# Performance work log

Measured on AMD Instinct MI355X. Metric: run time of the kernel, lower is better.

Reference implementation:

```python
import jax, jax.numpy as jnp
import numpy as np

D_IN = 768
D_OUT = 768
NUM_HEADS = 12
HEAD_DIM = D_OUT // NUM_HEADS


def setup_inputs() -> dict:
    key = jax.random.key(0)
    ks = jax.random.split(key, 9)
    s = 1.0 / np.sqrt(D_IN)
    x = jax.random.normal(ks[0], (8, 1024, D_IN), dtype=jnp.float32)
    Wq = jax.random.uniform(ks[1], (D_IN, D_OUT), jnp.float32, -s, s)
    Wk = jax.random.uniform(ks[2], (D_IN, D_OUT), jnp.float32, -s, s)
    Wv = jax.random.uniform(ks[3], (D_IN, D_OUT), jnp.float32, -s, s)
    Wo = jax.random.uniform(ks[4], (D_OUT, D_OUT), jnp.float32, -s, s)
    bq = jax.random.uniform(ks[5], (D_OUT,), jnp.float32, -s, s)
    bk = jax.random.uniform(ks[6], (D_OUT,), jnp.float32, -s, s)
    bv = jax.random.uniform(ks[7], (D_OUT,), jnp.float32, -s, s)
    bo = jax.random.uniform(ks[8], (D_OUT,), jnp.float32, -s, s)
    return {"x": x, "Wq": Wq, "bq": bq, "Wk": Wk, "bk": bk,
            "Wv": Wv, "bv": bv, "Wo": Wo, "bo": bo}


def reference(x, Wq, bq, Wk, bk, Wv, bv, Wo, bo):
    b, n, _ = x.shape
    # projections -> (b, heads, n, head_dim)
    def split_heads(t):
        return t.reshape(b, n, NUM_HEADS, HEAD_DIM).transpose(0, 2, 1, 3)
    q = split_heads(x @ Wq + bq)
    k = split_heads(x @ Wk + bk)
    v = split_heads(x @ Wv + bv)
    scale = 1.0 / jnp.sqrt(jnp.float32(HEAD_DIM)).astype(x.dtype)
    scores = jnp.einsum('bhqd,bhkd->bhqk', q, k) * scale
    attn = jax.nn.softmax(scores, axis=-1)  # dropout p=0.0 -> identity
    ctx = jnp.einsum('bhqk,bhkd->bhqd', attn, v)
    ctx = ctx.transpose(0, 2, 1, 3).reshape(b, n, D_OUT)
    return ctx @ Wo + bo
```

## Files before the change

### kernel.cpp

```cpp
#include <hip/hip_runtime.h>
#include <math.h>

#define D_MODEL 768
#define NHEAD  12
#define HDIM   64
#define SEQ    1024
#define BATCH  8
#define MTOT   (BATCH*SEQ)
#define QKV_N  2304
#define QK_LD  1536

typedef _Float16 f16;
typedef __attribute__((ext_vector_type(2))) __fp16 fp16x2;
typedef __attribute__((ext_vector_type(4))) _Float16 f16x4;
typedef __attribute__((ext_vector_type(8))) _Float16 f16x8;
typedef __attribute__((ext_vector_type(4))) float f32x4;
typedef __attribute__((ext_vector_type(16))) float f32x16;

union PFrag { unsigned u[4]; f16x8 v; };
union PackW { fp16x2 h; unsigned u; };

__device__ inline void gload_lds16(const void* g, void* l) {
    __builtin_amdgcn_global_load_lds(
        (const __attribute__((address_space(1))) void*)g,
        (__attribute__((address_space(3))) void*)l, 16, 0, 0);
}

__global__ __launch_bounds__(256) void prepass(
    const float* __restrict__ x, f16* __restrict__ xh, int n8,
    const float* __restrict__ bq, const float* __restrict__ bk,
    const float* __restrict__ bv, float* __restrict__ bqkv,
    const float* __restrict__ Wq, const float* __restrict__ Wk,
    const float* __restrict__ Wv, const float* __restrict__ Wo,
    f16* __restrict__ Wqkv_t, f16* __restrict__ Wo_t)
{
    __shared__ f16 tile[64][72];
    const int t = threadIdx.x;

    if (blockIdx.x < 3072) {
        const int i = blockIdx.x * 256 + t;
        if (i < n8) {
            const float4 a = *(const float4*)(x + (size_t)i * 8);
            const float4 b = *(const float4*)(x + (size_t)i * 8 + 4);
            f16x8 v;
            v[0] = (f16)a.x; v[1] = (f16)a.y; v[2] = (f16)a.z; v[3] = (f16)a.w;
            v[4] = (f16)b.x; v[5] = (f16)b.y; v[6] = (f16)b.z; v[7] = (f16)b.w;
            *(f16x8*)(xh + (size_t)i * 8) = v;
        }
        if (i < QKV_N)
            bqkv[i] = (i < 768) ? bq[i] : (i < 1536) ? bk[i - 768] : bv[i - 1536];
    } else {
        const int idx = blockIdx.x - 3072;
        const int z   = idx / 144;
        const int rem = idx % 144;
        const int k0  = (rem / 12) * 64;
        const int n0  = (rem % 12) * 64;
        const float* src = (z == 0) ? Wq : (z == 1) ? Wk : (z == 2) ? Wv : Wo;
        f16* dst = (z < 3) ? (Wqkv_t + (size_t)z * 768 * 768) : Wo_t;

        {
            const int r  = t >> 4;
            const int c4 = (t & 15) * 4;
            #pragma unroll
            for (int u = 0; u < 4; ++u) {
                const int row = r + u * 16;
                const float4 a = *(const float4*)&src[(size_t)(k0 + row) * 768 + n0 + c4];
                tile[row][c4 + 0] = (f16)a.x;
                tile[row][c4 + 1] = (f16)a.y;
                tile[row][c4 + 2] = (f16)a.z;
                tile[row][c4 + 3] = (f16)a.w;
            }
        }
        __syncthreads();
        {
            const int rn = t >> 3;
            const int ck = (t & 7) * 8;
            #pragma unroll
            for (int u = 0; u < 2; ++u) {
                const int n = rn + u * 32;
                f16x8 v;
                #pragma unroll
                for (int q = 0; q < 8; ++q) v[q] = tile[ck + q][n];
                *(f16x8*)&dst[(size_t)(n0 + n) * 768 + k0 + ck] = v;
            }
        }
    }
}

template<typename OUT_T, bool SPLITV, int BN>
__global__ __launch_bounds__(256) void gemm_f16_tn(
    const f16* __restrict__ A, const f16* __restrict__ Bt,
    const float* __restrict__ bias, OUT_T* __restrict__ C,
    f16* __restrict__ Vt,
    int M, int N, int K, int nb, int ldc)
{
    constexpr int NJ = BN / 32;
    __shared__ f16 As[128 * 64];
    __shared__ f16 Bs[BN * 64];

    const int t    = threadIdx.x;
    const int l15  = (t & 63) & 15;
    const int lg   = (t & 63) >> 4;
    const int w    = t >> 6;
    const int wrow = (w >> 1) * 64;
    const int wcol = (w & 1) * (BN / 2);

    const int orig = blockIdx.x;
    const int cpx  = gridDim.x >> 3;
    const int nid  = (orig & 7) * cpx + (orig >> 3);
    const int row0 = (nid / nb) * 128;
    const int col0 = (nid % nb) * BN;

    int src_row[4], src_koff[4], lds_off[4];
    #pragma unroll
    for (int i = 0; i < 4; ++i) {
        const int c = t + 256 * i;
        const int r = c >> 3;
        src_row[i]  = r;
        src_koff[i] = ((((c & 7) - (r >> 1)) & 7)) * 8;
        lds_off[i]  = c * 16;
    }

    int a_off[4][2], b_off[NJ][2];
    #pragma unroll
    for (int i = 0; i < 4; ++i) {
        const int ra = wrow + i * 16 + l15;
        #pragma unroll
        for (int s = 0; s < 2; ++s)
            a_off[i][s] = ra * 128 + (((s * 4 + lg + (ra >> 1)) & 7) * 16);
    }
    #pragma unroll
    for (int j = 0; j < NJ; ++j) {
        const int rb = wcol + j * 16 + l15;
        #pragma unroll
        for (int s = 0; s < 2; ++s)
            b_off[j][s] = rb * 128 + (((s * 4 + lg + (rb >> 1)) & 7) * 16);
    }

    f32x4 acc[4][NJ];
    #pragma unroll
    for (int i = 0; i < 4; ++i)
        #pragma unroll
        for (int j = 0; j < NJ; ++j)
            acc[i][j] = (f32x4){0.f, 0.f, 0.f, 0.f};

    const f16* Abase = A  + (size_t)row0 * K;
    const f16* Bbase = Bt + (size_t)col0 * K;

    for (int k0 = 0; k0 < K; k0 += 64) {
        #pragma unroll
        for (int i = 0; i < 4; ++i)
            gload_lds16(Abase + (size_t)src_row[i] * K + k0 + src_koff[i],
                        (char*)As + lds_off[i]);
        #pragma unroll
        for (int i = 0; i < BN / 32; ++i)
            gload_lds16(Bbase + (size_t)src_row[i] * K + k0 + src_koff[i],
                        (char*)Bs + lds_off[i]);
        __syncthreads();

        #pragma unroll
        for (int s = 0; s < 2; ++s) {
            f16x8 af[4], bf[NJ];
            #pragma unroll
            for (int i = 0; i < 4; ++i)
                af[i] = *(const f16x8*)((const char*)As + a_off[i][s]);
            #pragma unroll
            for (int j = 0; j < NJ; ++j)
                bf[j] = *(const f16x8*)((const char*)Bs + b_off[j][s]);
            #pragma unroll
            for (int i = 0; i < 4; ++i)
                #pragma unroll
                for (int j = 0; j < NJ; ++j)
                    acc[i][j] = __builtin_amdgcn_mfma_f32_16x16x32_f16(
                        af[i], bf[j], acc[i][j], 0, 0, 0);
        }
        __syncthreads();
    }

    #pragma unroll
    for (int j = 0; j < NJ; ++j) {
        const int col = col0 + wcol + j * 16 + l15;
        const float bj = bias[col];
        if (!SPLITV || col < 1536) {
            #pragma unroll
            for (int i = 0; i < 4; ++i) {
                const int row = row0 + wrow + i * 16 + lg * 4;
                #pragma unroll
                for (int q = 0; q < 4; ++q)
                    C[(size_t)(row + q) * ldc + col] = (OUT_T)(acc[i][j][q] + bj);
            }
        } else if (SPLITV) {
            const int h2 = (col - 1536) >> 6;
            const int d  = (col - 1536) & 63;
            #pragma unroll
            for (int i = 0; i < 4; ++i) {
                const int row = row0 + wrow + i * 16 + lg * 4;
                const int bb  = row >> 10;
                const int tok = row & 1023;
                f16x4 v4;
                #pragma unroll
                for (int q = 0; q < 4; ++q) v4[q] = (f16)(acc[i][j][q] + bj);
                *(f16x4*)(Vt + (((size_t)(bb * NHEAD + h2)) * 64 + d) * SEQ + tok) = v4;
            }
        }
    }
}

#define QMAP(r, hh) (((r) & 3) + 8 * ((r) >> 2) + 4 * (hh))

__global__ __launch_bounds__(256, 3) void attn_f16(
    const f16* __restrict__ QK, const f16* __restrict__ Vt,
    f16* __restrict__ O)
{
    __shared__ f16 KsB[2][64 * 64];
    __shared__ f16 VtB[2][64 * 64];

    const int t   = threadIdx.x;
    const int w   = t >> 6;
    const int l   = t & 63;
    const int l31 = l & 31;
    const int h   = l >> 5;
    const int sl  = (l & 7) << 4;

    const int orig = blockIdx.x;
    const int s    = (orig & 7) * 96 + (orig >> 3);
    const int bh   = s >> 3;
    const int qb   = s & 7;
    const int b  = bh / NHEAD;
    const int hd = bh % NHEAD;
    const int q0 = qb * 128;

    const size_t rowbase = (size_t)b * SEQ;
    const int qcol = hd * HDIM;

    const f16 hsc = (f16)(0.125f * 1.4426950408889634f);
    f16x8 qf[4];
    #pragma unroll
    for (int dc = 0; dc < 4; ++dc) {
        f16x8 v = *(const f16x8*)(QK
            + (rowbase + q0 + w * 32 + l31) * QK_LD
            + qcol + dc * 16 + h * 8);
        #pragma unroll
        for (int j = 0; j < 8; ++j) v[j] *= hsc;
        qf[dc] = v;
    }

    f32x16 ctx[2];
    #pragma unroll
    for (int dt = 0; dt < 2; ++dt)
        #pragma unroll
        for (int r = 0; r < 16; ++r) ctx[dt][r] = 0.f;
    float lsum = 0.f;

    const int rsub   = l >> 3;
    const int schunk = (l & 7) ^ rsub;
    const f16* ksrc = QK + (rowbase + w * 16 + rsub) * QK_LD
                         + 768 + qcol + schunk * 8;
    const f16* vsrc = Vt + (((size_t)bh * 64) + w * 16 + rsub) * SEQ
                         + schunk * 8;
    const size_t kstep = (size_t)64 * QK_LD;
    const int    woff  = w * 2048;

    gload_lds16(ksrc,             (char*)KsB[0] + woff);
    gload_lds16(ksrc + 8 * QK_LD, (char*)KsB[0] + woff + 1024);
    gload_lds16(vsrc,             (char*)VtB[0] + woff);
    gload_lds16(vsrc + 8 * SEQ,   (char*)VtB[0] + woff + 1024);
    __syncthreads();

    for (int kt = 0; kt < SEQ / 64; ++kt) {
        const int p = kt & 1;

        if (kt < SEQ / 64 - 1) {
            const f16* ks = ksrc + (size_t)(kt + 1) * kstep;
            const f16* vs = vsrc + (kt + 1) * 64;
            gload_lds16(ks,             (char*)KsB[p ^ 1] + woff);
            gload_lds16(ks + 8 * QK_LD, (char*)KsB[p ^ 1] + woff + 1024);
            gload_lds16(vs,             (char*)VtB[p ^ 1] + woff);
            gload_lds16(vs + 8 * SEQ,   (char*)VtB[p ^ 1] + woff + 1024);
        }

        const char* Kp = (const char*)KsB[p];
        const char* Vp = (const char*)VtB[p];

        f32x16 sacc[2];
        __builtin_amdgcn_s_setprio(1);
        #pragma unroll
        for (int kk = 0; kk < 2; ++kk) {
            f32x16 a;
            #pragma unroll
            for (int r = 0; r < 16; ++r) a[r] = 0.f;
            #pragma unroll
            for (int dc = 0; dc < 4; ++dc) {
                const f16x8 ka = *(const f16x8*)(Kp + (kk * 32 + l31) * 128
                                                    + ((dc * 32 + h * 16) ^ sl));
                a = __builtin_amdgcn_mfma_f32_32x32x16_f16(ka, qf[dc], a, 0, 0, 0);
            }
            sacc[kk] = a;
        }
        __builtin_amdgcn_s_setprio(0);

        {
            float ps0 = 0.f, ps1 = 0.f, ps2 = 0.f, ps3 = 0.f;
            #pragma unroll
            for (int kk = 0; kk < 2; ++kk)
                #pragma unroll
                for (int r = 0; r < 16; r += 4) {
                    const float e0 = exp2f(sacc[kk][r + 0]);
                    const float e1 = exp2f(sacc[kk][r + 1]);
                    const float e2 = exp2f(sacc[kk][r + 2]);
                    const float e3 = exp2f(sacc[kk][r + 3]);
                    sacc[kk][r + 0] = e0; ps0 += e0;
                    sacc[kk][r + 1] = e1; ps1 += e1;
                    sacc[kk][r + 2] = e2; ps2 += e2;
                    sacc[kk][r + 3] = e3; ps3 += e3;
                }
            lsum += (ps0 + ps1) + (ps2 + ps3);
        }

        unsigned paw[4][4];
        #pragma unroll
        for (int kk = 0; kk < 2; ++kk) {
            unsigned dw[8];
            #pragma unroll
            for (int i = 0; i < 8; ++i) {
                PackW u;
                u.h = __builtin_amdgcn_cvt_pkrtz(sacc[kk][2 * i], sacc[kk][2 * i + 1]);
                dw[i] = u.u;
            }
            const unsigned t0 = (unsigned)__shfl_xor((int)(h ? dw[0] : dw[2]), 32);
            const unsigned t1 = (unsigned)__shfl_xor((int)(h ? dw[1] : dw[3]), 32);
            const unsigned t2 = (unsigned)__shfl_xor((int)(h ? dw[4] : dw[6]), 32);
            const unsigned t3 = (unsigned)__shfl_xor((int)(h ? dw[5] : dw[7]), 32);
            paw[2 * kk][0]     = h ? t0    : dw[0];
            paw[2 * kk][1]     = h ? t1    : dw[1];
            paw[2 * kk][2]     = h ? dw[2] : t0;
            paw[2 * kk][3]     = h ? dw[3] : t1;
            paw[2 * kk + 1][0] = h ? t2    : dw[4];
            paw[2 * kk + 1][1] = h ? t3    : dw[5];
            paw[2 * kk + 1][2] = h ? dw[6] : t2;
            paw[2 * kk + 1][3] = h ? dw[7] : t3;
        }

        __builtin_amdgcn_s_setprio(1);
        #pragma unroll
        for (int c = 0; c < 4; ++c) {
            PFrag pf;
            pf.u[0] = paw[c][0]; pf.u[1] = paw[c][1];
            pf.u[2] = paw[c][2]; pf.u[3] = paw[c][3];
            #pragma unroll
            for (int dt = 0; dt < 2; ++dt) {
                const f16x8 vb = *(const f16x8*)(Vp + (dt * 32 + l31) * 128
                                                    + ((c * 32 + h * 16) ^ sl));
                ctx[dt] = __builtin_amdgcn_mfma_f32_32x32x16_f16(pf.v, vb, ctx[dt], 0, 0, 0);
            }
        }
        __builtin_amdgcn_s_setprio(0);

        __syncthreads();
    }

    {
        const float ltot = lsum + __shfl_xor(lsum, 32);
        const float inv  = 1.0f / ltot;
        #pragma unroll
        for (int r = 0; r < 16; ++r) {
            const float iv = __shfl(inv, QMAP(r, h));
            const size_t row = rowbase + q0 + w * 32 + QMAP(r, h);
            O[row * D_MODEL + qcol + l31]      = (f16)(ctx[0][r] * iv);
            O[row * D_MODEL + qcol + 32 + l31] = (f16)(ctx[1][r] * iv);
        }
    }
}

extern "C" void kernel_launch(void* const* d_in, const int* in_sizes, int n_in,
                              void* d_out, int out_size, void* d_ws, size_t ws_size,
                              hipStream_t stream) {
    const float* x  = (const float*)d_in[0];
    const float* Wq = (const float*)d_in[1];
    const float* bq = (const float*)d_in[2];
    const float* Wk = (const float*)d_in[3];
    const float* bk = (const float*)d_in[4];
    const float* Wv = (const float*)d_in[5];
    const float* bv = (const float*)d_in[6];
    const float* Wo = (const float*)d_in[7];
    const float* bo = (const float*)d_in[8];
    float* out = (float*)d_out;

    char* ws = (char*)d_ws;
    f16*   QKb     = (f16*)(ws);
    f16*   Vt      = (f16*)(ws + 25165824);
    f16*   xh      = (f16*)(ws + 37748736);
    f16*   ctxh    = (f16*)(ws + 50331648);
    f16*   Wqkv_t  = (f16*)(ws + 62914560);
    f16*   Wo_t    = (f16*)(ws + 66453504);
    float* bqkv    = (float*)(ws + 67633152);

    hipLaunchKernelGGL(prepass, dim3(3648), dim3(256), 0, stream,
                       x, xh, MTOT * D_MODEL / 8, bq, bk, bv, bqkv,
                       Wq, Wk, Wv, Wo, Wqkv_t, Wo_t);

    hipLaunchKernelGGL((gemm_f16_tn<f16, true, 128>), dim3((QKV_N / 128) * (MTOT / 128)), dim3(256), 0, stream,
                       xh, Wqkv_t, bqkv, QKb, Vt, MTOT, QKV_N, D_MODEL, QKV_N / 128, QK_LD);

    hipLaunchKernelGGL(attn_f16, dim3((SEQ / 128) * BATCH * NHEAD), dim3(256), 0, stream,
                       QKb, Vt, ctxh);

    hipLaunchKernelGGL((gemm_f16_tn<float, false, 64>), dim3((D_MODEL / 64) * (MTOT / 128)), dim3(256), 0, stream,
                       ctxh, Wo_t, bo, out, (f16*)nullptr, MTOT, D_MODEL, D_MODEL, D_MODEL / 64, D_MODEL);
}
```

Baseline: 119.4 us.

## Split attention KV range into two halves and merge partials in a separate kernel

The attention kernel now launches twice as many blocks. Each block processes only half of the key/value sequence and writes unnormalized f16 partial contexts plus row sums into reused workspace buffers. A new elementwise merge kernel adds the two partials and divides by the combined row sum. The aim is more parallelism and shorter per-block serial loops, at the cost of extra global traffic for the partials and one more kernel launch. The merge is only correct if the softmax uses no per-half running max.

```diff
diff --git a/kernel.cpp b/kernel.cpp
--- a/kernel.cpp
+++ b/kernel.cpp
@@ -9,6 +9,7 @@
 #define MTOT   (BATCH*SEQ)
 #define QKV_N  2304
 #define QK_LD  1536
+#define NBH    (BATCH*NHEAD)
 
 typedef _Float16 f16;
 typedef __attribute__((ext_vector_type(2))) __fp16 fp16x2;
@@ -210,7 +211,7 @@
 
 __global__ __launch_bounds__(256, 3) void attn_f16(
     const f16* __restrict__ QK, const f16* __restrict__ Vt,
-    f16* __restrict__ O)
+    f16* __restrict__ PA, f16* __restrict__ PB, float* __restrict__ L)
 {
     __shared__ f16 KsB[2][64 * 64];
     __shared__ f16 VtB[2][64 * 64];
@@ -223,9 +224,10 @@
     const int sl  = (l & 7) << 4;
 
     const int orig = blockIdx.x;
-    const int s    = (orig & 7) * 96 + (orig >> 3);
-    const int bh   = s >> 3;
-    const int qb   = s & 7;
+    const int s    = (orig & 7) * 192 + (orig >> 3);
+    const int bh   = s >> 4;
+    const int qb   = (s >> 1) & 7;
+    const int half = s & 1;
     const int b  = bh / NHEAD;
     const int hd = bh % NHEAD;
     const int q0 = qb * 128;
@@ -254,12 +256,12 @@
 
     const int rsub   = l >> 3;
     const int schunk = (l & 7) ^ rsub;
+    const size_t kstep = (size_t)64 * QK_LD;
     const f16* ksrc = QK + (rowbase + w * 16 + rsub) * QK_LD
-                         + 768 + qcol + schunk * 8;
+                         + 768 + qcol + schunk * 8 + (size_t)(half * 8) * kstep;
     const f16* vsrc = Vt + (((size_t)bh * 64) + w * 16 + rsub) * SEQ
-                         + schunk * 8;
-    const size_t kstep = (size_t)64 * QK_LD;
-    const int    woff  = w * 2048;
+                         + schunk * 8 + half * 8 * 64;
+    const int woff = w * 2048;
 
     gload_lds16(ksrc,             (char*)KsB[0] + woff);
     gload_lds16(ksrc + 8 * QK_LD, (char*)KsB[0] + woff + 1024);
@@ -267,10 +269,10 @@
     gload_lds16(vsrc + 8 * SEQ,   (char*)VtB[0] + woff + 1024);
     __syncthreads();
 
-    for (int kt = 0; kt < SEQ / 64; ++kt) {
+    for (int kt = 0; kt < 8; ++kt) {
         const int p = kt & 1;
 
-        if (kt < SEQ / 64 - 1) {
+        if (kt < 7) {
             const f16* ks = ksrc + (size_t)(kt + 1) * kstep;
             const f16* vs = vsrc + (kt + 1) * 64;
             gload_lds16(ks,             (char*)KsB[p ^ 1] + woff);
@@ -361,15 +363,39 @@
 
     {
         const float ltot = lsum + __shfl_xor(lsum, 32);
-        const float inv  = 1.0f / ltot;
+        if (h == 0)
+            L[(size_t)half * (NBH * SEQ) + bh * SEQ + q0 + w * 32 + l31] = ltot;
+        f16* Od = half ? PB : PA;
         #pragma unroll
         for (int r = 0; r < 16; ++r) {
-            const float iv = __shfl(inv, QMAP(r, h));
             const size_t row = rowbase + q0 + w * 32 + QMAP(r, h);
-            O[row * D_MODEL + qcol + l31]      = (f16)(ctx[0][r] * iv);
-            O[row * D_MODEL + qcol + 32 + l31] = (f16)(ctx[1][r] * iv);
-        }
-    }
+            Od[row * D_MODEL + qcol + l31]      = (f16)ctx[0][r];
+            Od[row * D_MODEL + qcol + 32 + l31] = (f16)ctx[1][r];
+        }
+    }
+}
+
+__global__ __launch_bounds__(256) void merge_halves(
+    const f16* __restrict__ PA, f16* __restrict__ PB,
+    const float* __restrict__ L)
+{
+    const int i   = blockIdx.x * 256 + threadIdx.x;
+    const int c8  = i % 96;
+    const int row = i / 96;
+    const int h   = c8 >> 3;
+    const int b   = row >> 10;
+    const int tok = row & 1023;
+    const int bh  = b * NHEAD + h;
+    const float la = L[bh * SEQ + tok];
+    const float lb = L[NBH * SEQ + bh * SEQ + tok];
+    const float inv = 1.0f / (la + lb);
+    const f16x8 a = *(const f16x8*)(PA + (size_t)i * 8);
+    const f16x8 c = *(const f16x8*)(PB + (size_t)i * 8);
+    f16x8 o;
+    #pragma unroll
+    for (int j = 0; j < 8; ++j)
+        o[j] = (f16)(((float)a[j] + (float)c[j]) * inv);
+    *(f16x8*)(PB + (size_t)i * 8) = o;
 }
 
 extern "C" void kernel_launch(void* const* d_in, const int* in_sizes, int n_in,
@@ -394,6 +420,7 @@
     f16*   Wqkv_t  = (f16*)(ws + 62914560);
     f16*   Wo_t    = (f16*)(ws + 66453504);
     float* bqkv    = (float*)(ws + 67633152);
+    float* Lbuf    = (float*)Wqkv_t;
 
     hipLaunchKernelGGL(prepass, dim3(3648), dim3(256), 0, stream,
                        x, xh, MTOT * D_MODEL / 8, bq, bk, bv, bqkv,
@@ -402,8 +429,11 @@
     hipLaunchKernelGGL((gemm_f16_tn<f16, true, 128>), dim3((QKV_N / 128) * (MTOT / 128)), dim3(256), 0, stream,
                        xh, Wqkv_t, bqkv, QKb, Vt, MTOT, QKV_N, D_MODEL, QKV_N / 128, QK_LD);
 
-    hipLaunchKernelGGL(attn_f16, dim3((SEQ / 128) * BATCH * NHEAD), dim3(256), 0, stream,
-                       QKb, Vt, ctxh);
+    hipLaunchKernelGGL(attn_f16, dim3(2 * (SEQ / 128) * NBH), dim3(256), 0, stream,
+                       QKb, Vt, xh, ctxh, Lbuf);
+
+    hipLaunchKernelGGL(merge_halves, dim3(MTOT * D_MODEL / 8 / 256), dim3(256), 0, stream,
+                       xh, ctxh, Lbuf);
 
     hipLaunchKernelGGL((gemm_f16_tn<float, false, 64>), dim3((D_MODEL / 64) * (MTOT / 128)), dim3(256), 0, stream,
                        ctxh, Wo_t, bo, out, (f16*)nullptr, MTOT, D_MODEL, D_MODEL, D_MODEL / 64, D_MODEL);
```

Result: slower. 125.2 us (+4.8%).
